# Kernel optimization log

Measured on AMD Instinct MI355X. Metric: run time of the kernel, lower is better.

Reference implementation:

```python
import jax, jax.numpy as jnp
import numpy as np

B, PS, H, W = 32, 1536, 32, 64
TNS = H * W                 # total_num_selects = 2048
NJ = TNS // 16              # num_joints = 128
QK = PS // 4                # q/k channels = 384
NC = 200                    # num_classes
BN_EPS = 1e-5


def setup_inputs() -> dict:
    key = jax.random.key(0)
    ks = jax.random.split(key, 8)
    s = 0.02  # small init scale for weights
    inp = {
        "x": jax.random.normal(ks[0], (B, PS, H, W), jnp.float32),
        # param_pool0: Linear(TNS -> NJ)
        "w_pool0": jax.random.normal(ks[1], (NJ, TNS), jnp.float32) * s,
        "b_pool0": jnp.zeros((NJ,), jnp.float32),
        # learnable adjacency: eye/100 + 1/100
        "adj1": jnp.eye(NJ, dtype=jnp.float32) / 100.0 + 1.0 / 100.0,
        # conv_q1 / conv_k1: Conv1d(PS -> PS//4, kernel=1)
        "w_q": jax.random.normal(ks[2], (QK, PS), jnp.float32) * s,
        "b_q": jnp.zeros((QK,), jnp.float32),
        "w_k": jax.random.normal(ks[3], (QK, PS), jnp.float32) * s,
        "b_k": jnp.zeros((QK,), jnp.float32),
        # alpha1 (torch inits to 0; we use 0.1 so attention branch has nonzero effect/grads)
        "alpha": jnp.array([0.1], jnp.float32),
        # conv1: Conv1d(PS -> PS, kernel=1)
        "w_c1": jax.random.normal(ks[4], (PS, PS), jnp.float32) * s,
        "b_c1": jnp.zeros((PS,), jnp.float32),
        # batch_norm1 affine params
        "gamma": jnp.ones((PS,), jnp.float32),
        "beta": jnp.zeros((PS,), jnp.float32),
        # param_pool1: Linear(NJ -> 1)
        "w_pool1": jax.random.normal(ks[5], (1, NJ), jnp.float32) * s,
        "b_pool1": jnp.zeros((1,), jnp.float32),
        # classifier: Linear(PS -> NC)
        "w_cls": jax.random.normal(ks[6], (NC, PS), jnp.float32) * s,
        "b_cls": jnp.zeros((NC,), jnp.float32),
    }
    return inp


def reference(x, w_pool0, b_pool0, adj1, w_q, b_q, w_k, b_k, alpha,
              w_c1, b_c1, gamma, beta, w_pool1, b_pool1, w_cls, b_cls):
    b, c = x.shape[0], x.shape[1]
    hs = x.reshape(b, c, -1)                                   # (B, PS, TNS)
    # param_pool0: pool selects down to joints
    hs = jnp.einsum('bcs,js->bcj', hs, w_pool0) + b_pool0      # (B, PS, NJ)
    # 1x1-conv q/k then mean over channel dim
    q1 = (jnp.einsum('oc,bcj->boj', w_q, hs) + b_q[:, None]).mean(axis=1)  # (B, NJ)
    k1 = (jnp.einsum('oc,bcj->boj', w_k, hs) + b_k[:, None]).mean(axis=1)  # (B, NJ)
    # outer-difference attention, tanh-bounded, blended with learnable adjacency
    A1 = adj1 + jnp.tanh(q1[:, :, None] - k1[:, None, :]) * alpha[0]       # (B, NJ, NJ)
    # conv1 (1x1) then adjacency-weighted matmul
    hs = jnp.einsum('oc,bcj->boj', w_c1, hs) + b_c1[:, None]   # (B, PS, NJ)
    hs = jnp.einsum('bcj,bjk->bck', hs, A1)                    # (B, PS, NJ)
    # BatchNorm1d over (batch, joints) per channel (training-mode batch stats)
    mean = hs.mean(axis=(0, 2))
    var = hs.var(axis=(0, 2))
    hs = (hs - mean[None, :, None]) * jax.lax.rsqrt(var + BN_EPS)[None, :, None]
    hs = gamma[None, :, None] * hs + beta[None, :, None]
    # param_pool1 (NJ -> 1), dropout is identity in eval, flatten, classify
    hs = jnp.einsum('bcj,j->bc', hs, w_pool1[0]) + b_pool1[0]  # (B, PS)
    out = hs @ w_cls.T + b_cls                                 # (B, NC)
    return out
```

## Files before the change

### kernel.cpp

```cpp
#include <hip/hip_runtime.h>
#include <hip/hip_bf16.h>

#define B_ 32
#define PS_ 1536
#define TNS_ 2048
#define NJ_ 128
#define QK_ 384
#define NC_ 200
#define BN_EPS_ 1e-5f

typedef __attribute__((ext_vector_type(8))) short short8;
typedef __attribute__((ext_vector_type(4))) float float4v;
typedef unsigned short ushort_t;

__device__ __forceinline__ unsigned short f2b(float f) {
    unsigned int u = __float_as_uint(f);
    return (unsigned short)((u + 0x7FFFu + ((u >> 16) & 1u)) >> 16);
}
__device__ __forceinline__ float b2f_lo(unsigned int u) { return __uint_as_float(u << 16); }
__device__ __forceinline__ float b2f_hi(unsigned int u) { return __uint_as_float(u & 0xffff0000u); }

__device__ __forceinline__ void mma_chunk(const short* As, const short* Bs,
                                          int wm, int wn, int lane, float4v acc[4][4]) {
    const int m0 = wm + (lane & 15);
    const int n0 = wn + (lane & 15);
    const int quad = lane >> 4;
    #pragma unroll
    for (int kk = 0; kk < 64; kk += 32) {
        short8 a[4], b[4];
        const int kb = quad * 8 + kk;
        #pragma unroll
        for (int i = 0; i < 4; ++i) {
            a[i] = *(const short8*)&As[(m0 + i * 16) * 72 + kb];
            b[i] = *(const short8*)&Bs[(n0 + i * 16) * 72 + kb];
        }
        #pragma unroll
        for (int i = 0; i < 4; ++i)
            #pragma unroll
            for (int j = 0; j < 4; ++j)
                acc[i][j] = __builtin_amdgcn_mfma_f32_16x16x32_bf16(a[i], b[j], acc[i][j], 0, 0, 0);
    }
}

__device__ __forceinline__ void stage_f32(const float* __restrict__ src, size_t stride,
                                          short* dst, int tid) {
    #pragma unroll
    for (int p = 0; p < 8; ++p) {
        int r = (tid >> 4) + p * 16;
        int kq = (tid & 15) * 4;
        float4 v = *(const float4*)(src + (size_t)r * stride + kq);
        ushort4 u = { f2b(v.x), f2b(v.y), f2b(v.z), f2b(v.w) };
        *(ushort4*)&dst[r * 72 + kq] = u;
    }
}
__device__ __forceinline__ void stage_b16(const ushort_t* __restrict__ src, size_t stride,
                                          short* dst, int tid) {
    #pragma unroll
    for (int p = 0; p < 4; ++p) {
        int r = (tid >> 3) + p * 32;
        int kq = (tid & 7) * 8;
        uint4 v = *(const uint4*)(src + (size_t)r * stride + kq);
        *(uint4*)&dst[r * 72 + kq] = v;
    }
}

__global__ void k_prep(const float* __restrict__ wq, const float* __restrict__ bq,
                       const float* __restrict__ wk, const float* __restrict__ bk,
                       const float* __restrict__ wp1,
                       float* __restrict__ wqb, float* __restrict__ wkb,
                       float* __restrict__ scal) {
    const int blk = blockIdx.x;
    const int tid = threadIdx.x;
    if (blk < 6) {
        int c = blk * 256 + tid;
        float s = 0.f;
        for (int o = 0; o < QK_; ++o) s += wq[(size_t)o * PS_ + c];
        wqb[c] = s * (1.0f / QK_);
    } else if (blk < 12) {
        int c = (blk - 6) * 256 + tid;
        float s = 0.f;
        for (int o = 0; o < QK_; ++o) s += wk[(size_t)o * PS_ + c];
        wkb[c] = s * (1.0f / QK_);
    } else {
        __shared__ float red[256];
        float s = (tid < QK_ ? bq[tid] : 0.f) + (tid + 256 < QK_ ? bq[tid + 256] : 0.f);
        red[tid] = s; __syncthreads();
        for (int off = 128; off > 0; off >>= 1) { if (tid < off) red[tid] += red[tid + off]; __syncthreads(); }
        if (tid == 0) scal[0] = red[0] * (1.0f / QK_);
        __syncthreads();
        s = (tid < QK_ ? bk[tid] : 0.f) + (tid + 256 < QK_ ? bk[tid + 256] : 0.f);
        red[tid] = s; __syncthreads();
        for (int off = 128; off > 0; off >>= 1) { if (tid < off) red[tid] += red[tid + off]; __syncthreads(); }
        if (tid == 0) scal[1] = red[0] * (1.0f / QK_);
        __syncthreads();
        s = (tid < NJ_ ? wp1[tid] : 0.f);
        red[tid] = s; __syncthreads();
        for (int off = 128; off > 0; off >>= 1) { if (tid < off) red[tid] += red[tid + off]; __syncthreads(); }
        if (tid == 0) scal[2] = red[0];
    }
}

__global__ void k_f2b4(const float* __restrict__ src, ushort_t* __restrict__ dst, int n4) {
    int i = blockIdx.x * 256 + threadIdx.x;
    if (i < n4) {
        float4 v = ((const float4*)src)[i];
        ushort4 u = { f2b(v.x), f2b(v.y), f2b(v.z), f2b(v.w) };
        ((ushort4*)dst)[i] = u;
    }
}

__global__ __launch_bounds__(256) void k_gemm1(const float* __restrict__ x,
        const ushort_t* __restrict__ w0b, const float* __restrict__ b0,
        ushort_t* __restrict__ hsT) {
    __shared__ __align__(16) short As[128 * 72];
    __shared__ __align__(16) short Bs[128 * 72];
    const int tid = threadIdx.x, lane = tid & 63, wave = tid >> 6;
    const int wm = (wave >> 1) * 64, wn = (wave & 1) * 64;
    const size_t m0 = (size_t)blockIdx.x * 128;
    float4v acc[4][4] = {};
    for (int k0 = 0; k0 < TNS_; k0 += 64) {
        stage_f32(x + m0 * TNS_ + k0, TNS_, As, tid);
        stage_b16(w0b + k0, TNS_, Bs, tid);
        __syncthreads();
        mma_chunk(As, Bs, wm, wn, lane, acc);
        __syncthreads();
    }
    const int b = blockIdx.x / 12, cb = (blockIdx.x % 12) * 128;
    const int quad = lane >> 4;
    #pragma unroll
    for (int jn = 0; jn < 4; ++jn) {
        int j = wn + jn * 16 + (lane & 15);
        float bj = b0[j];
        #pragma unroll
        for (int im = 0; im < 4; ++im) {
            int c = cb + wm + im * 16 + quad * 4;
            float4v v = acc[im][jn];
            ushort4 u = { f2b(v[0] + bj), f2b(v[1] + bj), f2b(v[2] + bj), f2b(v[3] + bj) };
            *(ushort4*)&hsT[((size_t)(b * NJ_ + j)) * PS_ + c] = u;
        }
    }
}

__global__ __launch_bounds__(256) void k_q1k1(const ushort_t* __restrict__ hsT,
        const float* __restrict__ wqb, const float* __restrict__ wkb,
        float* __restrict__ q1, float* __restrict__ k1) {
    int wid = blockIdx.x * 4 + (threadIdx.x >> 6);
    int lane = threadIdx.x & 63;
    int b = wid >> 7, j = wid & 127;
    const unsigned int* row = (const unsigned int*)(hsT + ((size_t)(b * NJ_ + j)) * PS_);
    float sq = 0.f, sk = 0.f;
    #pragma unroll
    for (int i = 0; i < 12; ++i) {
        unsigned int u = row[i * 64 + lane];
        int c = (i * 64 + lane) * 2;
        float v0 = b2f_lo(u), v1 = b2f_hi(u);
        sq += wqb[c] * v0 + wqb[c + 1] * v1;
        sk += wkb[c] * v0 + wkb[c + 1] * v1;
    }
    #pragma unroll
    for (int off = 32; off > 0; off >>= 1) { sq += __shfl_down(sq, off, 64); sk += __shfl_down(sk, off, 64); }
    if (lane == 0) { q1[b * NJ_ + j] = sq; k1[b * NJ_ + j] = sk; }
}

__global__ void k_a1(const float* __restrict__ adj, const float* __restrict__ q1,
                     const float* __restrict__ k1, const float* __restrict__ alpha,
                     const float* __restrict__ scal, ushort_t* __restrict__ A1t) {
    int idx = blockIdx.x * 256 + threadIdx.x;
    int b = idx >> 14;
    int r = idx & 16383;
    int j2 = r >> 7;
    int j = r & 127;
    float dbias = scal[0] - scal[1];
    float t = tanhf(q1[b * NJ_ + j] - k1[b * NJ_ + j2] + dbias);
    A1t[idx] = f2b(adj[j * NJ_ + j2] + t * alpha[0]);
}

__global__ __launch_bounds__(256) void k_gemm2(const ushort_t* __restrict__ wc1b,
        const float* __restrict__ bc1, const ushort_t* __restrict__ hsT,
        ushort_t* __restrict__ hs2) {
    __shared__ __align__(16) short As[128 * 72];
    __shared__ __align__(16) short Bs[128 * 72];
    const int tid = threadIdx.x, lane = tid & 63, wave = tid >> 6;
    const int wm = (wave >> 1) * 64, wn = (wave & 1) * 64;
    const int b = blockIdx.y, ob = blockIdx.x * 128;
    float4v acc[4][4] = {};
    const ushort_t* Abase = wc1b + (size_t)ob * PS_;
    const ushort_t* Bbase = hsT + (size_t)b * NJ_ * PS_;
    for (int k0 = 0; k0 < PS_; k0 += 64) {
        stage_b16(Abase + k0, PS_, As, tid);
        stage_b16(Bbase + k0, PS_, Bs, tid);
        __syncthreads();
        mma_chunk(As, Bs, wm, wn, lane, acc);
        __syncthreads();
    }
    const int quad = lane >> 4;
    #pragma unroll
    for (int im = 0; im < 4; ++im) {
        int o0 = ob + wm + im * 16 + quad * 4;
        float bc[4] = { bc1[o0], bc1[o0 + 1], bc1[o0 + 2], bc1[o0 + 3] };
        #pragma unroll
        for (int jn = 0; jn < 4; ++jn) {
            int j = wn + jn * 16 + (lane & 15);
            float4v v = acc[im][jn];
            #pragma unroll
            for (int r = 0; r < 4; ++r)
                hs2[((size_t)(b * PS_) + o0 + r) * NJ_ + j] = f2b(v[r] + bc[r]);
        }
    }
}

__global__ __launch_bounds__(256) void k_gemm3(const ushort_t* __restrict__ hs2,
        const ushort_t* __restrict__ A1t, ushort_t* __restrict__ hs3b) {
    __shared__ __align__(16) short As[128 * 72];
    __shared__ __align__(16) short Bs[128 * 72];
    const int tid = threadIdx.x, lane = tid & 63, wave = tid >> 6;
    const int wm = (wave >> 1) * 64, wn = (wave & 1) * 64;
    const int b = blockIdx.y, cbs = blockIdx.x * 128;
    float4v acc[4][4] = {};
    const ushort_t* Abase = hs2 + ((size_t)(b * PS_) + cbs) * NJ_;
    const ushort_t* Bbase = A1t + (size_t)b * NJ_ * NJ_;
    for (int k0 = 0; k0 < NJ_; k0 += 64) {
        stage_b16(Abase + k0, NJ_, As, tid);
        stage_b16(Bbase + k0, NJ_, Bs, tid);
        __syncthreads();
        mma_chunk(As, Bs, wm, wn, lane, acc);
        __syncthreads();
    }
    const int quad = lane >> 4;
    #pragma unroll
    for (int im = 0; im < 4; ++im) {
        int c0 = cbs + wm + im * 16 + quad * 4;
        #pragma unroll
        for (int jn = 0; jn < 4; ++jn) {
            int j2 = wn + jn * 16 + (lane & 15);
            float4v v = acc[im][jn];
            #pragma unroll
            for (int r = 0; r < 4; ++r)
                hs3b[((size_t)(b * PS_) + c0 + r) * NJ_ + j2] = f2b(v[r]);
        }
    }
}

__global__ void k_bnstats(const ushort_t* __restrict__ hs3b,
                          float* __restrict__ bnsum, float* __restrict__ bnsq) {
    int c = blockIdx.x, tid = threadIdx.x;
    float s = 0.f, q = 0.f;
    for (int b = 0; b < B_; ++b) {
        float v = __uint_as_float(((unsigned int)hs3b[((size_t)(b * PS_) + c) * NJ_ + tid]) << 16);
        s += v; q += v * v;
    }
    __shared__ float ss[2], qq[2];
    #pragma unroll
    for (int off = 32; off > 0; off >>= 1) { s += __shfl_down(s, off, 64); q += __shfl_down(q, off, 64); }
    int w = tid >> 6;
    if ((tid & 63) == 0) { ss[w] = s; qq[w] = q; }
    __syncthreads();
    if (tid == 0) { bnsum[c] = ss[0] + ss[1]; bnsq[c] = qq[0] + qq[1]; }
}

__global__ void k_pool(const ushort_t* __restrict__ hs3b, const float* __restrict__ bnsum,
                       const float* __restrict__ bnsq, const float* __restrict__ gamma,
                       const float* __restrict__ beta, const float* __restrict__ wp1,
                       const float* __restrict__ bp1, const float* __restrict__ scal,
                       float* __restrict__ p) {
    int gid = blockIdx.x * 256 + threadIdx.x;
    int row = gid >> 6;
    int lane = gid & 63;
    int c = row % PS_;
    const unsigned int* hp = (const unsigned int*)(hs3b + (size_t)row * NJ_);
    unsigned int u = hp[lane];
    float d = wp1[2 * lane] * b2f_lo(u) + wp1[2 * lane + 1] * b2f_hi(u);
    #pragma unroll
    for (int off = 32; off > 0; off >>= 1) d += __shfl_down(d, off, 64);
    if (lane == 0) {
        float mean = bnsum[c] * (1.0f / 4096.0f);
        float var = bnsq[c] * (1.0f / 4096.0f) - mean * mean;
        float s = gamma[c] * rsqrtf(var + BN_EPS_);
        p[row] = s * d + (beta[c] - s * mean) * scal[2] + bp1[0];
    }
}

__global__ void k_cls(const float* __restrict__ p, const float* __restrict__ wcls,
                      const float* __restrict__ bcls, float* __restrict__ out) {
    int gid = blockIdx.x * 256 + threadIdx.x;
    int w = gid >> 6;
    int lane = gid & 63;
    int b = w / 200, n = w % 200;
    const float* pp = p + (size_t)b * PS_;
    const float* wp = wcls + (size_t)n * PS_;
    float s = 0.f;
    for (int c = lane; c < PS_; c += 64) s += pp[c] * wp[c];
    #pragma unroll
    for (int off = 32; off > 0; off >>= 1) s += __shfl_down(s, off, 64);
    if (lane == 0) out[w] = s + bcls[n];
}

extern "C" void kernel_launch(void* const* d_in, const int* in_sizes, int n_in,
                              void* d_out, int out_size, void* d_ws, size_t ws_size,
                              hipStream_t stream) {
    const float* x       = (const float*)d_in[0];
    const float* w_pool0 = (const float*)d_in[1];
    const float* b_pool0 = (const float*)d_in[2];
    const float* adj1    = (const float*)d_in[3];
    const float* w_q     = (const float*)d_in[4];
    const float* b_q     = (const float*)d_in[5];
    const float* w_k     = (const float*)d_in[6];
    const float* b_k     = (const float*)d_in[7];
    const float* alpha   = (const float*)d_in[8];
    const float* w_c1    = (const float*)d_in[9];
    const float* b_c1    = (const float*)d_in[10];
    const float* gamma   = (const float*)d_in[11];
    const float* beta    = (const float*)d_in[12];
    const float* w_pool1 = (const float*)d_in[13];
    const float* b_pool1 = (const float*)d_in[14];
    const float* w_cls   = (const float*)d_in[15];
    const float* b_cls   = (const float*)d_in[16];
    float* out = (float*)d_out;

    ushort_t* hsT  = (ushort_t*)d_ws;
    ushort_t* hs2  = hsT + 6291456;
    ushort_t* hs3b = hs2 + 6291456;
    ushort_t* w0b  = hs3b + 6291456;
    ushort_t* wc1b = w0b + 262144;
    ushort_t* A1t  = wc1b + 2359296;
    float* fb    = (float*)(A1t + 524288);
    float* wqb   = fb;
    float* wkb   = wqb + 1536;
    float* scal  = wkb + 1536;
    float* q1    = scal + 16;
    float* k1    = q1 + 4096;
    float* bnsum = k1 + 4096;
    float* bnsq  = bnsum + 1536;
    float* pbuf  = bnsq + 1536;
    size_t need = 44040192u + (size_t)(1536 + 1536 + 16 + 4096 + 4096 + 1536 + 1536 + 49152) * 4;
    if (ws_size < need) return;

    k_prep <<<13, 256, 0, stream>>>(w_q, b_q, w_k, b_k, w_pool1, wqb, wkb, scal);
    k_f2b4 <<<256, 256, 0, stream>>>(w_pool0, w0b, 65536);
    k_f2b4 <<<2304, 256, 0, stream>>>(w_c1, wc1b, 589824);
    k_gemm1<<<384, 256, 0, stream>>>(x, w0b, b_pool0, hsT);
    k_q1k1 <<<1024, 256, 0, stream>>>(hsT, wqb, wkb, q1, k1);
    k_a1   <<<2048, 256, 0, stream>>>(adj1, q1, k1, alpha, scal, A1t);
    k_gemm2<<<dim3(12, 32), 256, 0, stream>>>(wc1b, b_c1, hsT, hs2);
    k_gemm3<<<dim3(12, 32), 256, 0, stream>>>(hs2, A1t, hs3b);
    k_bnstats<<<1536, 128, 0, stream>>>(hs3b, bnsum, bnsq);
    k_pool <<<12288, 256, 0, stream>>>(hs3b, bnsum, bnsq, gamma, beta, w_pool1, b_pool1, scal, pbuf);
    k_cls  <<<1600, 256, 0, stream>>>(pbuf, w_cls, b_cls, out);
}
```

Measured before the change: 689.7 us.

## Register-prefetch GEMM tiles, fuse BN stats into gemm3, merge prep kernels

```diff
diff --git a/kernel.cpp b/kernel.cpp
--- a/kernel.cpp
+++ b/kernel.cpp
@@ -42,33 +42,49 @@
     }
 }
 
-__device__ __forceinline__ void stage_f32(const float* __restrict__ src, size_t stride,
-                                          short* dst, int tid) {
+__device__ __forceinline__ void load_f32(const float* __restrict__ src, size_t stride,
+                                         int tid, float4 r[8]) {
     #pragma unroll
     for (int p = 0; p < 8; ++p) {
-        int r = (tid >> 4) + p * 16;
+        int row = (tid >> 4) + p * 16;
         int kq = (tid & 15) * 4;
-        float4 v = *(const float4*)(src + (size_t)r * stride + kq);
-        ushort4 u = { f2b(v.x), f2b(v.y), f2b(v.z), f2b(v.w) };
-        *(ushort4*)&dst[r * 72 + kq] = u;
-    }
-}
-__device__ __forceinline__ void stage_b16(const ushort_t* __restrict__ src, size_t stride,
-                                          short* dst, int tid) {
+        r[p] = *(const float4*)(src + (size_t)row * stride + kq);
+    }
+}
+__device__ __forceinline__ void write_f32(const float4 r[8], short* dst, int tid) {
+    #pragma unroll
+    for (int p = 0; p < 8; ++p) {
+        int row = (tid >> 4) + p * 16;
+        int kq = (tid & 15) * 4;
+        ushort4 u = { f2b(r[p].x), f2b(r[p].y), f2b(r[p].z), f2b(r[p].w) };
+        *(ushort4*)&dst[row * 72 + kq] = u;
+    }
+}
+__device__ __forceinline__ void load_b16(const ushort_t* __restrict__ src, size_t stride,
+                                         int tid, uint4 r[4]) {
     #pragma unroll
     for (int p = 0; p < 4; ++p) {
-        int r = (tid >> 3) + p * 32;
+        int row = (tid >> 3) + p * 32;
         int kq = (tid & 7) * 8;
-        uint4 v = *(const uint4*)(src + (size_t)r * stride + kq);
-        *(uint4*)&dst[r * 72 + kq] = v;
-    }
-}
-
-__global__ void k_prep(const float* __restrict__ wq, const float* __restrict__ bq,
-                       const float* __restrict__ wk, const float* __restrict__ bk,
-                       const float* __restrict__ wp1,
-                       float* __restrict__ wqb, float* __restrict__ wkb,
-                       float* __restrict__ scal) {
+        r[p] = *(const uint4*)(src + (size_t)row * stride + kq);
+    }
+}
+__device__ __forceinline__ void write_b16(const uint4 r[4], short* dst, int tid) {
+    #pragma unroll
+    for (int p = 0; p < 4; ++p) {
+        int row = (tid >> 3) + p * 32;
+        int kq = (tid & 7) * 8;
+        *(uint4*)&dst[row * 72 + kq] = r[p];
+    }
+}
+
+__global__ void k_prep_all(const float* __restrict__ wq, const float* __restrict__ bq,
+                           const float* __restrict__ wk, const float* __restrict__ bk,
+                           const float* __restrict__ wp1,
+                           const float* __restrict__ w_pool0, const float* __restrict__ w_c1,
+                           float* __restrict__ wqb, float* __restrict__ wkb,
+                           float* __restrict__ scal,
+                           ushort_t* __restrict__ w0b, ushort_t* __restrict__ wc1b) {
     const int blk = blockIdx.x;
     const int tid = threadIdx.x;
     if (blk < 6) {
@@ -81,7 +97,7 @@
         float s = 0.f;
         for (int o = 0; o < QK_; ++o) s += wk[(size_t)o * PS_ + c];
         wkb[c] = s * (1.0f / QK_);
-    } else {
+    } else if (blk == 12) {
         __shared__ float red[256];
         float s = (tid < QK_ ? bq[tid] : 0.f) + (tid + 256 < QK_ ? bq[tid + 256] : 0.f);
         red[tid] = s; __syncthreads();
@@ -97,15 +113,16 @@
         red[tid] = s; __syncthreads();
         for (int off = 128; off > 0; off >>= 1) { if (tid < off) red[tid] += red[tid + off]; __syncthreads(); }
         if (tid == 0) scal[2] = red[0];
-    }
-}
-
-__global__ void k_f2b4(const float* __restrict__ src, ushort_t* __restrict__ dst, int n4) {
-    int i = blockIdx.x * 256 + threadIdx.x;
-    if (i < n4) {
-        float4 v = ((const float4*)src)[i];
+    } else if (blk < 13 + 256) {
+        int i = (blk - 13) * 256 + tid;
+        float4 v = ((const float4*)w_pool0)[i];
         ushort4 u = { f2b(v.x), f2b(v.y), f2b(v.z), f2b(v.w) };
-        ((ushort4*)dst)[i] = u;
+        ((ushort4*)w0b)[i] = u;
+    } else {
+        int i = (blk - 269) * 256 + tid;
+        float4 v = ((const float4*)w_c1)[i];
+        ushort4 u = { f2b(v.x), f2b(v.y), f2b(v.z), f2b(v.w) };
+        ((ushort4*)wc1b)[i] = u;
     }
 }
 
@@ -118,10 +135,18 @@
     const int wm = (wave >> 1) * 64, wn = (wave & 1) * 64;
     const size_t m0 = (size_t)blockIdx.x * 128;
     float4v acc[4][4] = {};
+    float4 aR[8];
+    uint4  bR[4];
+    load_f32(x + m0 * TNS_, TNS_, tid, aR);
+    load_b16(w0b, TNS_, tid, bR);
     for (int k0 = 0; k0 < TNS_; k0 += 64) {
-        stage_f32(x + m0 * TNS_ + k0, TNS_, As, tid);
-        stage_b16(w0b + k0, TNS_, Bs, tid);
-        __syncthreads();
+        write_f32(aR, As, tid);
+        write_b16(bR, Bs, tid);
+        __syncthreads();
+        if (k0 + 64 < TNS_) {
+            load_f32(x + m0 * TNS_ + k0 + 64, TNS_, tid, aR);
+            load_b16(w0b + k0 + 64, TNS_, tid, bR);
+        }
         mma_chunk(As, Bs, wm, wn, lane, acc);
         __syncthreads();
     }
@@ -186,10 +211,17 @@
     float4v acc[4][4] = {};
     const ushort_t* Abase = wc1b + (size_t)ob * PS_;
     const ushort_t* Bbase = hsT + (size_t)b * NJ_ * PS_;
+    uint4 aR[4], bR[4];
+    load_b16(Abase, PS_, tid, aR);
+    load_b16(Bbase, PS_, tid, bR);
     for (int k0 = 0; k0 < PS_; k0 += 64) {
-        stage_b16(Abase + k0, PS_, As, tid);
-        stage_b16(Bbase + k0, PS_, Bs, tid);
-        __syncthreads();
+        write_b16(aR, As, tid);
+        write_b16(bR, Bs, tid);
+        __syncthreads();
+        if (k0 + 64 < PS_) {
+            load_b16(Abase + k0 + 64, PS_, tid, aR);
+            load_b16(Bbase + k0 + 64, PS_, tid, bR);
+        }
         mma_chunk(As, Bs, wm, wn, lane, acc);
         __syncthreads();
     }
@@ -210,7 +242,8 @@
 }
 
 __global__ __launch_bounds__(256) void k_gemm3(const ushort_t* __restrict__ hs2,
-        const ushort_t* __restrict__ A1t, ushort_t* __restrict__ hs3b) {
+        const ushort_t* __restrict__ A1t, ushort_t* __restrict__ hs3b,
+        float* __restrict__ bnsum, float* __restrict__ bnsq) {
     __shared__ __align__(16) short As[128 * 72];
     __shared__ __align__(16) short Bs[128 * 72];
     const int tid = threadIdx.x, lane = tid & 63, wave = tid >> 6;
@@ -219,10 +252,17 @@
     float4v acc[4][4] = {};
     const ushort_t* Abase = hs2 + ((size_t)(b * PS_) + cbs) * NJ_;
     const ushort_t* Bbase = A1t + (size_t)b * NJ_ * NJ_;
+    uint4 aR[4], bR[4];
+    load_b16(Abase, NJ_, tid, aR);
+    load_b16(Bbase, NJ_, tid, bR);
     for (int k0 = 0; k0 < NJ_; k0 += 64) {
-        stage_b16(Abase + k0, NJ_, As, tid);
-        stage_b16(Bbase + k0, NJ_, Bs, tid);
-        __syncthreads();
+        write_b16(aR, As, tid);
+        write_b16(bR, Bs, tid);
+        __syncthreads();
+        if (k0 + 64 < NJ_) {
+            load_b16(Abase + k0 + 64, NJ_, tid, aR);
+            load_b16(Bbase + k0 + 64, NJ_, tid, bR);
+        }
         mma_chunk(As, Bs, wm, wn, lane, acc);
         __syncthreads();
     }
@@ -230,32 +270,34 @@
     #pragma unroll
     for (int im = 0; im < 4; ++im) {
         int c0 = cbs + wm + im * 16 + quad * 4;
+        float s[4] = {0.f, 0.f, 0.f, 0.f}, q[4] = {0.f, 0.f, 0.f, 0.f};
         #pragma unroll
         for (int jn = 0; jn < 4; ++jn) {
             int j2 = wn + jn * 16 + (lane & 15);
             float4v v = acc[im][jn];
             #pragma unroll
-            for (int r = 0; r < 4; ++r)
+            for (int r = 0; r < 4; ++r) {
                 hs3b[((size_t)(b * PS_) + c0 + r) * NJ_ + j2] = f2b(v[r]);
-        }
-    }
-}
-
-__global__ void k_bnstats(const ushort_t* __restrict__ hs3b,
-                          float* __restrict__ bnsum, float* __restrict__ bnsq) {
-    int c = blockIdx.x, tid = threadIdx.x;
-    float s = 0.f, q = 0.f;
-    for (int b = 0; b < B_; ++b) {
-        float v = __uint_as_float(((unsigned int)hs3b[((size_t)(b * PS_) + c) * NJ_ + tid]) << 16);
-        s += v; q += v * v;
-    }
-    __shared__ float ss[2], qq[2];
-    #pragma unroll
-    for (int off = 32; off > 0; off >>= 1) { s += __shfl_down(s, off, 64); q += __shfl_down(q, off, 64); }
-    int w = tid >> 6;
-    if ((tid & 63) == 0) { ss[w] = s; qq[w] = q; }
-    __syncthreads();
-    if (tid == 0) { bnsum[c] = ss[0] + ss[1]; bnsq[c] = qq[0] + qq[1]; }
+                s[r] += v[r];
+                q[r] += v[r] * v[r];
+            }
+        }
+        #pragma unroll
+        for (int r = 0; r < 4; ++r) {
+            #pragma unroll
+            for (int off = 8; off > 0; off >>= 1) {
+                s[r] += __shfl_down(s[r], off, 16);
+                q[r] += __shfl_down(q[r], off, 16);
+            }
+        }
+        if ((lane & 15) == 0) {
+            #pragma unroll
+            for (int r = 0; r < 4; ++r) {
+                atomicAdd(&bnsum[c0 + r], s[r]);
+                atomicAdd(&bnsq[c0 + r], q[r]);
+            }
+        }
+    }
 }
 
 __global__ void k_pool(const ushort_t* __restrict__ hs3b, const float* __restrict__ bnsum,
@@ -335,15 +377,15 @@
     size_t need = 44040192u + (size_t)(1536 + 1536 + 16 + 4096 + 4096 + 1536 + 1536 + 49152) * 4;
     if (ws_size < need) return;
 
-    k_prep <<<13, 256, 0, stream>>>(w_q, b_q, w_k, b_k, w_pool1, wqb, wkb, scal);
-    k_f2b4 <<<256, 256, 0, stream>>>(w_pool0, w0b, 65536);
-    k_f2b4 <<<2304, 256, 0, stream>>>(w_c1, wc1b, 589824);
+    hipMemsetAsync((void*)bnsum, 0, (1536 + 1536) * sizeof(float), stream);
+
+    k_prep_all<<<2573, 256, 0, stream>>>(w_q, b_q, w_k, b_k, w_pool1, w_pool0, w_c1,
+                                         wqb, wkb, scal, w0b, wc1b);
     k_gemm1<<<384, 256, 0, stream>>>(x, w0b, b_pool0, hsT);
     k_q1k1 <<<1024, 256, 0, stream>>>(hsT, wqb, wkb, q1, k1);
     k_a1   <<<2048, 256, 0, stream>>>(adj1, q1, k1, alpha, scal, A1t);
     k_gemm2<<<dim3(12, 32), 256, 0, stream>>>(wc1b, b_c1, hsT, hs2);
-    k_gemm3<<<dim3(12, 32), 256, 0, stream>>>(hs2, A1t, hs3b);
-    k_bnstats<<<1536, 128, 0, stream>>>(hs3b, bnsum, bnsq);
+    k_gemm3<<<dim3(12, 32), 256, 0, stream>>>(hs2, A1t, hs3b, bnsum, bnsq);
     k_pool <<<12288, 256, 0, stream>>>(hs3b, bnsum, bnsq, gamma, beta, w_pool1, b_pool1, scal, pbuf);
     k_cls  <<<1600, 256, 0, stream>>>(pbuf, w_cls, b_cls, out);
 }
```

After: 789.7 us. +14.5%, slower.
